# Optimization experiments

Hardware: AMD Instinct MI355X
Metric: run time of the kernel (lower is better)

The kernel has to match this reference:

```python
import jax, jax.numpy as jnp
import numpy as np

N_DOMAINS = 8
LN_EPS = 1e-5


def setup_inputs() -> dict:
    key = jax.random.key(0)
    ks = jax.random.split(key, 4)
    N, D_IN, D_HID, D_OUT = 32768, 256, 1024, 256
    x = jax.random.normal(ks[0], (N, D_IN), dtype=jnp.float32)
    domain_types = jax.random.randint(ks[1], (N,), 0, N_DOMAINS, dtype=jnp.int32)
    # Per-domain MLP parameters (8 independent experts)
    W1 = jax.random.normal(ks[2], (N_DOMAINS, D_IN, D_HID), dtype=jnp.float32) * (1.0 / np.sqrt(D_IN))
    b1 = jnp.zeros((N_DOMAINS, D_HID), dtype=jnp.float32)
    gamma = jnp.ones((N_DOMAINS, D_HID), dtype=jnp.float32)
    beta = jnp.zeros((N_DOMAINS, D_HID), dtype=jnp.float32)
    W2 = jax.random.normal(ks[3], (N_DOMAINS, D_HID, D_OUT), dtype=jnp.float32) * (1.0 / np.sqrt(D_HID))
    b2 = jnp.zeros((N_DOMAINS, D_OUT), dtype=jnp.float32)
    return {"x": x, "domain_types": domain_types, "W1": W1, "b1": b1,
            "gamma": gamma, "beta": beta, "W2": W2, "b2": b2}


def _expert_mlp(x, W1d, b1d, gd, bd, W2d, b2d):
    # Linear -> LayerNorm -> ReLU -> (Dropout: identity at eval) -> Linear
    h = x @ W1d + b1d                       # [N, hid]
    mu = jnp.mean(h, axis=-1, keepdims=True)
    var = jnp.mean(jnp.square(h - mu), axis=-1, keepdims=True)
    h = (h - mu) * jax.lax.rsqrt(var + LN_EPS) * gd + bd
    h = jax.nn.relu(h)
    return h @ W2d + b2d                    # [N, out]


def reference(x, domain_types, W1, b1, gamma, beta, W2, b2):
    # output dim == x.shape[-1] (as in the torch code: zeros(batch, x.shape[-1]))
    out = jnp.zeros((x.shape[0], x.shape[-1]), dtype=x.dtype)
    for d in range(N_DOMAINS):  # small fixed expert loop (static MoE dispatch)
        y = _expert_mlp(x, W1[d], b1[d], gamma[d], beta[d], W2[d], b2[d])
        mask = (domain_types == d)[:, None]
        out = jnp.where(mask, y, out)
    return out
```

## Files before the change

### kernel.cpp

```cpp
#include <hip/hip_runtime.h>
#include <hip/hip_bf16.h>


#define ND 8
#define NROWS 32768
#define DIN 256
#define DHID 1024
#define DOUT 256
#define MPAD 33792
#define NTILES 264

typedef short short8 __attribute__((ext_vector_type(8)));
typedef float floatx4 __attribute__((ext_vector_type(4)));

__device__ __forceinline__ unsigned short f2bf(float f) {
    unsigned u = __builtin_bit_cast(unsigned, f);
    unsigned r = u + 0x7fff + ((u >> 16) & 1);
    return (unsigned short)(r >> 16);
}
__device__ __forceinline__ float bf2f(unsigned short h) {
    unsigned u = ((unsigned)h) << 16;
    return __builtin_bit_cast(float, u);
}

#define GLDS16(gp, lp) __builtin_amdgcn_global_load_lds( \
    (const __attribute__((address_space(1))) void*)(gp), \
    (__attribute__((address_space(3))) void*)(lp), 16, 0, 0)

__global__ void transpose_bf16(const float* __restrict__ in,
                               unsigned short* __restrict__ out,
                               int R, int C) {
    __shared__ float t[32][33];
    const int z = blockIdx.z;
    const int c0 = blockIdx.x * 32, r0 = blockIdx.y * 32;
    const int tx = threadIdx.x & 31, ty = threadIdx.x >> 5;
    const float* src = in + (size_t)z * R * C;
    unsigned short* dst = out + (size_t)z * R * C;
#pragma unroll
    for (int i = 0; i < 32; i += 8)
        t[ty + i][tx] = src[(size_t)(r0 + ty + i) * C + c0 + tx];
    __syncthreads();
#pragma unroll
    for (int i = 0; i < 32; i += 8)
        dst[(size_t)(c0 + ty + i) * R + r0 + tx] = f2bf(t[tx][ty + i]);
}

__global__ void zero_init(int* __restrict__ perm, int* __restrict__ rowdom,
                          int* __restrict__ cnt) {
    int i = blockIdx.x * 256 + threadIdx.x;
    if (i < MPAD) { perm[i] = -1; rowdom[i] = 0; }
    if (i < 16) cnt[i] = 0;
}

__global__ void histo(const int* __restrict__ dt, int* __restrict__ counts) {
    __shared__ int lc[ND];
    if (threadIdx.x < ND) lc[threadIdx.x] = 0;
    __syncthreads();
    int i = blockIdx.x * 256 + threadIdx.x;
    atomicAdd(&lc[dt[i]], 1);
    __syncthreads();
    if (threadIdx.x < ND) atomicAdd(&counts[threadIdx.x], lc[threadIdx.x]);
}

__global__ void make_meta(const int* __restrict__ counts, int* __restrict__ cursors,
                          int2* __restrict__ meta) {
    if (threadIdx.x == 0 && blockIdx.x == 0) {
        int off = 0, t = 0;
        for (int d = 0; d < ND; d++) {
            cursors[d] = off;
            int nt = (counts[d] + 127) >> 7;
            for (int i = 0; i < nt; i++) meta[t++] = make_int2(d, off + (i << 7));
            off += nt << 7;
        }
        for (; t < NTILES; t++) meta[t] = make_int2(-1, 0);
    }
}

__global__ __launch_bounds__(256)
void assign_pos(const int* __restrict__ dt, int* __restrict__ cursors,
                int* __restrict__ perm, int* __restrict__ rowdom,
                int* __restrict__ pos) {
    __shared__ int lcnt[ND];
    __shared__ int lbase[ND];
    const int tid = threadIdx.x;
    if (tid < ND) lcnt[tid] = 0;
    __syncthreads();
    const int r = blockIdx.x * 256 + tid;
    const int d = dt[r];
    const int myrank = atomicAdd(&lcnt[d], 1);
    __syncthreads();
    if (tid < ND && lcnt[tid] > 0)
        lbase[tid] = atomicAdd(&cursors[tid], lcnt[tid]);
    __syncthreads();
    const int p = lbase[d] + myrank;
    pos[r] = p;
    perm[p] = r;
    rowdom[p] = d;
}

__global__ __launch_bounds__(256)
void copy_rows(const float* __restrict__ x, const int* __restrict__ pos,
               unsigned short* __restrict__ xs) {
    const int tid = threadIdx.x;
    const int lane = tid & 63;
    const int r = blockIdx.x * 4 + (tid >> 6);
    const int p = pos[r];
    float4 v = ((const float4*)(x + (size_t)r * DIN))[lane];
    ushort4 o;
    o.x = f2bf(v.x); o.y = f2bf(v.y); o.z = f2bf(v.z); o.w = f2bf(v.w);
    ((ushort4*)(xs + (size_t)p * DIN))[lane] = o;
}

template <int K, bool SCATTER>
__global__ __launch_bounds__(256, 2)
void gemm_bt(const unsigned short* __restrict__ A,
             const unsigned short* __restrict__ Bt,
             const float* __restrict__ bias,
             const int2* __restrict__ meta,
             const int* __restrict__ perm,
             unsigned short* __restrict__ Cbf,
             float* __restrict__ Cf,
             const int Ntot) {
    const int2 md = meta[blockIdx.x];
    const int dom = md.x;
    if (dom < 0) return;
    const int m0 = md.y;
    const int n0 = blockIdx.y * 128;

    __shared__ unsigned short As[128 * 32];
    __shared__ unsigned short Bs[128 * 32];

    const int tid = threadIdx.x;
    const int lane = tid & 63;
    const int w = tid >> 6;
    const int wr = w >> 1, wc = w & 1;

    const unsigned short* Abase = A + (size_t)m0 * K;
    const unsigned short* Bbase = Bt + (size_t)dom * Ntot * K + (size_t)n0 * K;

    floatx4 acc[4][4];
#pragma unroll
    for (int i = 0; i < 4; i++)
#pragma unroll
        for (int j = 0; j < 4; j++) acc[i][j] = 0.f;

    for (int k0 = 0; k0 < K; k0 += 32) {
#pragma unroll
        for (int it = 0; it < 2; ++it) {
            const int c = w * 128 + it * 64 + lane;
            const int m = c >> 2, kc = c & 3;
            GLDS16(Abase + (size_t)m * K + k0 + kc * 8, &As[(w * 128 + it * 64) * 8]);
            GLDS16(Bbase + (size_t)m * K + k0 + kc * 8, &Bs[(w * 128 + it * 64) * 8]);
        }
        __syncthreads();

        short8 a[4], b[4];
        const int kk = (lane >> 4) * 8;
#pragma unroll
        for (int i = 0; i < 4; i++) {
            const int m = wr * 64 + i * 16 + (lane & 15);
            a[i] = *(const short8*)&As[m * 32 + kk];
            const int n = wc * 64 + i * 16 + (lane & 15);
            b[i] = *(const short8*)&Bs[n * 32 + kk];
        }
#pragma unroll
        for (int i = 0; i < 4; i++)
#pragma unroll
            for (int j = 0; j < 4; j++)
                acc[i][j] = __builtin_amdgcn_mfma_f32_16x16x32_bf16(a[i], b[j], acc[i][j], 0, 0, 0);
        __syncthreads();
    }

    const int quad = lane >> 4;
#pragma unroll
    for (int i = 0; i < 4; i++) {
        const int rowbase = m0 + wr * 64 + i * 16 + quad * 4;
        if (!SCATTER) {
#pragma unroll
            for (int j = 0; j < 4; j++) {
                const int col = n0 + wc * 64 + j * 16 + (lane & 15);
                const float bv = bias[dom * Ntot + col];
#pragma unroll
                for (int r = 0; r < 4; r++)
                    Cbf[(size_t)(rowbase + r) * Ntot + col] = f2bf(acc[i][j][r] + bv);
            }
        } else {
#pragma unroll
            for (int r = 0; r < 4; r++) {
                const int orig = perm[rowbase + r];
                if (orig < 0) continue;
#pragma unroll
                for (int j = 0; j < 4; j++) {
                    const int col = n0 + wc * 64 + j * 16 + (lane & 15);
                    Cf[(size_t)orig * Ntot + col] = acc[i][j][r] + bias[dom * Ntot + col];
                }
            }
        }
    }
}

__global__ __launch_bounds__(256)
void ln_relu(unsigned short* __restrict__ H, const float* __restrict__ gamma,
             const float* __restrict__ beta, const int* __restrict__ rowdom) {
    const int row = blockIdx.x;
    const int tid = threadIdx.x;
    const int dom = rowdom[row];
    unsigned short* hr = H + (size_t)row * DHID;
    ushort4 raw = ((const ushort4*)hr)[tid];
    float v0 = bf2f(raw.x), v1 = bf2f(raw.y), v2 = bf2f(raw.z), v3 = bf2f(raw.w);
    float s = v0 + v1 + v2 + v3;
    float s2 = v0 * v0 + v1 * v1 + v2 * v2 + v3 * v3;
#pragma unroll
    for (int o = 32; o; o >>= 1) {
        s += __shfl_xor(s, o, 64);
        s2 += __shfl_xor(s2, o, 64);
    }
    __shared__ float red[8];
    const int w = tid >> 6;
    if ((tid & 63) == 0) { red[w] = s; red[4 + w] = s2; }
    __syncthreads();
    s = red[0] + red[1] + red[2] + red[3];
    s2 = red[4] + red[5] + red[6] + red[7];
    const float inv = 1.0f / 1024.0f;
    const float mu = s * inv;
    const float var = fmaxf(s2 * inv - mu * mu, 0.f);
    const float rstd = rsqrtf(var + 1e-5f);
    const float* g = gamma + dom * DHID + tid * 4;
    const float* b = beta + dom * DHID + tid * 4;
    ushort4 o4;
    o4.x = f2bf(fmaxf((v0 - mu) * rstd * g[0] + b[0], 0.f));
    o4.y = f2bf(fmaxf((v1 - mu) * rstd * g[1] + b[1], 0.f));
    o4.z = f2bf(fmaxf((v2 - mu) * rstd * g[2] + b[2], 0.f));
    o4.w = f2bf(fmaxf((v3 - mu) * rstd * g[3] + b[3], 0.f));
    ((ushort4*)hr)[tid] = o4;
}

extern "C" void kernel_launch(void* const* d_in, const int* in_sizes, int n_in,
                              void* d_out, int out_size, void* d_ws, size_t ws_size,
                              hipStream_t stream) {
    const float* x = (const float*)d_in[0];
    const int* dt = (const int*)d_in[1];
    const float* W1 = (const float*)d_in[2];
    const float* b1 = (const float*)d_in[3];
    const float* gamma = (const float*)d_in[4];
    const float* beta = (const float*)d_in[5];
    const float* W2 = (const float*)d_in[6];
    const float* b2 = (const float*)d_in[7];
    float* out = (float*)d_out;

    char* ws = (char*)d_ws;
    size_t off = 0;
    auto take = [&](size_t nbytes) -> char* {
        char* p = ws + off;
        off = (off + nbytes + 255) & ~(size_t)255;
        return p;
    };
    unsigned short* W1T = (unsigned short*)take((size_t)ND * DHID * DIN * 2);
    unsigned short* W2T = (unsigned short*)take((size_t)ND * DOUT * DHID * 2);
    unsigned short* XS  = (unsigned short*)take((size_t)MPAD * DIN * 2);
    unsigned short* H   = (unsigned short*)take((size_t)MPAD * DHID * 2);
    int* PERM   = (int*)take(MPAD * 4);
    int* ROWDOM = (int*)take(MPAD * 4);
    int* POS    = (int*)take(NROWS * 4);
    int* CNT    = (int*)take(64);
    int2* META  = (int2*)take(NTILES * 8);
    (void)ws_size; (void)n_in; (void)in_sizes; (void)out_size;

    int* COUNTS = CNT;
    int* CURSORS = CNT + 8;

    transpose_bf16<<<dim3(DHID / 32, DIN / 32, ND), 256, 0, stream>>>(W1, W1T, DIN, DHID);
    transpose_bf16<<<dim3(DOUT / 32, DHID / 32, ND), 256, 0, stream>>>(W2, W2T, DHID, DOUT);
    zero_init<<<(MPAD + 255) / 256, 256, 0, stream>>>(PERM, ROWDOM, CNT);
    histo<<<NROWS / 256, 256, 0, stream>>>(dt, COUNTS);
    make_meta<<<1, 1, 0, stream>>>(COUNTS, CURSORS, META);
    assign_pos<<<NROWS / 256, 256, 0, stream>>>(dt, CURSORS, PERM, ROWDOM, POS);
    copy_rows<<<NROWS / 4, 256, 0, stream>>>(x, POS, XS);
    gemm_bt<DIN, false><<<dim3(NTILES, DHID / 128), 256, 0, stream>>>(
        XS, W1T, b1, META, nullptr, H, nullptr, DHID);
    ln_relu<<<MPAD, 256, 0, stream>>>(H, gamma, beta, ROWDOM);
    gemm_bt<DHID, true><<<dim3(NTILES, DOUT / 128), 256, 0, stream>>>(
        H, W2T, b2, META, PERM, nullptr, out, DOUT);
}
```

Measured before the change: 227.4 us.

## Fuse first expert GEMM with LayerNorm+ReLU epilogue and drop zero-init kernel

Replaces the first GEMM and the separate LayerNorm/ReLU pass with one kernel. Each 512-thread block computes 64 rows across the full 1024 hidden columns, reduces mean and variance in the epilogue through shared memory, and writes the normalized bf16 activations once. This removes a full read-modify-write of the hidden buffer and a kernel launch. The zero_init kernel is also removed: counter reset moves into the transpose kernel and padding-row perm reset into make_meta. The wider block needs a large B tile in LDS (64 KB) and more accumulator registers, which may reduce occupancy. It also computes statistics from fp32 accumulators instead of bf16-rounded values.

```diff
diff --git a/kernel.cpp b/kernel.cpp
--- a/kernel.cpp
+++ b/kernel.cpp
@@ -29,11 +29,13 @@
 
 __global__ void transpose_bf16(const float* __restrict__ in,
                                unsigned short* __restrict__ out,
-                               int R, int C) {
+                               int R, int C, int* __restrict__ cnt) {
     __shared__ float t[32][33];
     const int z = blockIdx.z;
     const int c0 = blockIdx.x * 32, r0 = blockIdx.y * 32;
     const int tx = threadIdx.x & 31, ty = threadIdx.x >> 5;
+    if (cnt && blockIdx.x == 0 && blockIdx.y == 0 && z == 0 && threadIdx.x < 16)
+        cnt[threadIdx.x] = 0;
     const float* src = in + (size_t)z * R * C;
     unsigned short* dst = out + (size_t)z * R * C;
 #pragma unroll
@@ -43,13 +45,6 @@
 #pragma unroll
     for (int i = 0; i < 32; i += 8)
         dst[(size_t)(c0 + ty + i) * R + r0 + tx] = f2bf(t[tx][ty + i]);
-}
-
-__global__ void zero_init(int* __restrict__ perm, int* __restrict__ rowdom,
-                          int* __restrict__ cnt) {
-    int i = blockIdx.x * 256 + threadIdx.x;
-    if (i < MPAD) { perm[i] = -1; rowdom[i] = 0; }
-    if (i < 16) cnt[i] = 0;
 }
 
 __global__ void histo(const int* __restrict__ dt, int* __restrict__ counts) {
@@ -63,13 +58,14 @@
 }
 
 __global__ void make_meta(const int* __restrict__ counts, int* __restrict__ cursors,
-                          int2* __restrict__ meta) {
+                          int2* __restrict__ meta, int* __restrict__ perm) {
     if (threadIdx.x == 0 && blockIdx.x == 0) {
         int off = 0, t = 0;
         for (int d = 0; d < ND; d++) {
             cursors[d] = off;
             int nt = (counts[d] + 127) >> 7;
             for (int i = 0; i < nt; i++) meta[t++] = make_int2(d, off + (i << 7));
+            for (int p = off + counts[d]; p < off + (nt << 7); p++) perm[p] = -1;
             off += nt << 7;
         }
         for (; t < NTILES; t++) meta[t] = make_int2(-1, 0);
@@ -78,8 +74,7 @@
 
 __global__ __launch_bounds__(256)
 void assign_pos(const int* __restrict__ dt, int* __restrict__ cursors,
-                int* __restrict__ perm, int* __restrict__ rowdom,
-                int* __restrict__ pos) {
+                int* __restrict__ perm, int* __restrict__ pos) {
     __shared__ int lcnt[ND];
     __shared__ int lbase[ND];
     const int tid = threadIdx.x;
@@ -95,7 +90,6 @@
     const int p = lbase[d] + myrank;
     pos[r] = p;
     perm[p] = r;
-    rowdom[p] = d;
 }
 
 __global__ __launch_bounds__(256)
@@ -111,16 +105,141 @@
     ((ushort4*)(xs + (size_t)p * DIN))[lane] = o;
 }
 
-template <int K, bool SCATTER>
+__global__ __launch_bounds__(512, 2)
+void gemm_ln(const unsigned short* __restrict__ A,
+             const unsigned short* __restrict__ Bt,
+             const float* __restrict__ bias,
+             const float* __restrict__ gamma,
+             const float* __restrict__ beta,
+             const int2* __restrict__ meta,
+             unsigned short* __restrict__ H) {
+    const int2 md = meta[blockIdx.x >> 1];
+    const int dom = md.x;
+    if (dom < 0) return;
+    const int m0 = md.y + (blockIdx.x & 1) * 64;
+
+    __shared__ unsigned short As[64 * 32];
+    __shared__ unsigned short Bs[1024 * 32];
+    __shared__ float red_s[64][9];
+    __shared__ float red_q[64][9];
+    __shared__ float mu_s[64], rs_s[64];
+
+    const int tid = threadIdx.x;
+    const int lane = tid & 63;
+    const int w = tid >> 6;
+    const int c16 = lane & 15;
+    const int quad = lane >> 4;
+
+    const unsigned short* Abase = A + (size_t)m0 * DIN;
+    const unsigned short* Bbase = Bt + (size_t)dom * DHID * DIN;
+
+    floatx4 acc[4][8];
+#pragma unroll
+    for (int i = 0; i < 4; i++)
+#pragma unroll
+        for (int j = 0; j < 8; j++) acc[i][j] = 0.f;
+
+    for (int k0 = 0; k0 < DIN; k0 += 32) {
+#pragma unroll
+        for (int it = 0; it < 8; ++it) {
+            const int c = (w * 8 + it) * 64 + lane;
+            const int n = c >> 2, kc = c & 3;
+            GLDS16(Bbase + (size_t)n * DIN + k0 + kc * 8, &Bs[(w * 8 + it) * 512]);
+        }
+        if (w < 4) {
+            const int c = w * 64 + lane;
+            const int m = c >> 2, kc = c & 3;
+            GLDS16(Abase + (size_t)m * DIN + k0 + kc * 8, &As[w * 512]);
+        }
+        __syncthreads();
+
+        const int kk = quad * 8;
+        short8 a[4], b[8];
+#pragma unroll
+        for (int i = 0; i < 4; i++)
+            a[i] = *(const short8*)&As[(i * 16 + c16) * 32 + kk];
+#pragma unroll
+        for (int j = 0; j < 8; j++)
+            b[j] = *(const short8*)&Bs[(w * 128 + j * 16 + c16) * 32 + kk];
+#pragma unroll
+        for (int i = 0; i < 4; i++)
+#pragma unroll
+            for (int j = 0; j < 8; j++)
+                acc[i][j] = __builtin_amdgcn_mfma_f32_16x16x32_bf16(a[i], b[j], acc[i][j], 0, 0, 0);
+        __syncthreads();
+    }
+
+    float bv[8];
+#pragma unroll
+    for (int j = 0; j < 8; j++) bv[j] = bias[dom * DHID + w * 128 + j * 16 + c16];
+
+#pragma unroll
+    for (int i = 0; i < 4; i++) {
+#pragma unroll
+        for (int r = 0; r < 4; r++) {
+            float s = 0.f, q = 0.f;
+#pragma unroll
+            for (int j = 0; j < 8; j++) {
+                float v = acc[i][j][r] + bv[j];
+                acc[i][j][r] = v;
+                s += v; q += v * v;
+            }
+#pragma unroll
+            for (int o = 1; o < 16; o <<= 1) {
+                s += __shfl_xor(s, o, 64);
+                q += __shfl_xor(q, o, 64);
+            }
+            if (c16 == 0) {
+                const int row = i * 16 + quad * 4 + r;
+                red_s[row][w] = s;
+                red_q[row][w] = q;
+            }
+        }
+    }
+    __syncthreads();
+
+    if (tid < 64) {
+        float s = 0.f, q = 0.f;
+#pragma unroll
+        for (int ww = 0; ww < 8; ww++) { s += red_s[tid][ww]; q += red_q[tid][ww]; }
+        const float inv = 1.0f / (float)DHID;
+        const float mu = s * inv;
+        const float var = fmaxf(q * inv - mu * mu, 0.f);
+        mu_s[tid] = mu;
+        rs_s[tid] = rsqrtf(var + 1e-5f);
+    }
+    __syncthreads();
+
+    float gv[8], btv[8];
+#pragma unroll
+    for (int j = 0; j < 8; j++) {
+        gv[j] = gamma[dom * DHID + w * 128 + j * 16 + c16];
+        btv[j] = beta[dom * DHID + w * 128 + j * 16 + c16];
+    }
+#pragma unroll
+    for (int i = 0; i < 4; i++) {
+#pragma unroll
+        for (int r = 0; r < 4; r++) {
+            const int row = i * 16 + quad * 4 + r;
+            const float mu = mu_s[row], rs = rs_s[row];
+            unsigned short* hrow = H + (size_t)(m0 + row) * DHID + w * 128;
+#pragma unroll
+            for (int j = 0; j < 8; j++) {
+                float v = (acc[i][j][r] - mu) * rs * gv[j] + btv[j];
+                hrow[j * 16 + c16] = f2bf(fmaxf(v, 0.f));
+            }
+        }
+    }
+}
+
 __global__ __launch_bounds__(256, 2)
 void gemm_bt(const unsigned short* __restrict__ A,
              const unsigned short* __restrict__ Bt,
              const float* __restrict__ bias,
              const int2* __restrict__ meta,
              const int* __restrict__ perm,
-             unsigned short* __restrict__ Cbf,
              float* __restrict__ Cf,
-             const int Ntot) {
+             const int Ntot, const int K) {
     const int2 md = meta[blockIdx.x];
     const int dom = md.x;
     if (dom < 0) return;
@@ -175,64 +294,17 @@
 #pragma unroll
     for (int i = 0; i < 4; i++) {
         const int rowbase = m0 + wr * 64 + i * 16 + quad * 4;
-        if (!SCATTER) {
+#pragma unroll
+        for (int r = 0; r < 4; r++) {
+            const int orig = perm[rowbase + r];
+            if (orig < 0) continue;
 #pragma unroll
             for (int j = 0; j < 4; j++) {
                 const int col = n0 + wc * 64 + j * 16 + (lane & 15);
-                const float bv = bias[dom * Ntot + col];
-#pragma unroll
-                for (int r = 0; r < 4; r++)
-                    Cbf[(size_t)(rowbase + r) * Ntot + col] = f2bf(acc[i][j][r] + bv);
-            }
-        } else {
-#pragma unroll
-            for (int r = 0; r < 4; r++) {
-                const int orig = perm[rowbase + r];
-                if (orig < 0) continue;
-#pragma unroll
-                for (int j = 0; j < 4; j++) {
-                    const int col = n0 + wc * 64 + j * 16 + (lane & 15);
-                    Cf[(size_t)orig * Ntot + col] = acc[i][j][r] + bias[dom * Ntot + col];
-                }
-            }
-        }
-    }
-}
-
-__global__ __launch_bounds__(256)
-void ln_relu(unsigned short* __restrict__ H, const float* __restrict__ gamma,
-             const float* __restrict__ beta, const int* __restrict__ rowdom) {
-    const int row = blockIdx.x;
-    const int tid = threadIdx.x;
-    const int dom = rowdom[row];
-    unsigned short* hr = H + (size_t)row * DHID;
-    ushort4 raw = ((const ushort4*)hr)[tid];
-    float v0 = bf2f(raw.x), v1 = bf2f(raw.y), v2 = bf2f(raw.z), v3 = bf2f(raw.w);
-    float s = v0 + v1 + v2 + v3;
-    float s2 = v0 * v0 + v1 * v1 + v2 * v2 + v3 * v3;
-#pragma unroll
-    for (int o = 32; o; o >>= 1) {
-        s += __shfl_xor(s, o, 64);
-        s2 += __shfl_xor(s2, o, 64);
-    }
-    __shared__ float red[8];
-    const int w = tid >> 6;
-    if ((tid & 63) == 0) { red[w] = s; red[4 + w] = s2; }
-    __syncthreads();
-    s = red[0] + red[1] + red[2] + red[3];
-    s2 = red[4] + red[5] + red[6] + red[7];
-    const float inv = 1.0f / 1024.0f;
-    const float mu = s * inv;
-    const float var = fmaxf(s2 * inv - mu * mu, 0.f);
-    const float rstd = rsqrtf(var + 1e-5f);
-    const float* g = gamma + dom * DHID + tid * 4;
-    const float* b = beta + dom * DHID + tid * 4;
-    ushort4 o4;
-    o4.x = f2bf(fmaxf((v0 - mu) * rstd * g[0] + b[0], 0.f));
-    o4.y = f2bf(fmaxf((v1 - mu) * rstd * g[1] + b[1], 0.f));
-    o4.z = f2bf(fmaxf((v2 - mu) * rstd * g[2] + b[2], 0.f));
-    o4.w = f2bf(fmaxf((v3 - mu) * rstd * g[3] + b[3], 0.f));
-    ((ushort4*)hr)[tid] = o4;
+                Cf[(size_t)orig * Ntot + col] = acc[i][j][r] + bias[dom * Ntot + col];
+            }
+        }
+    }
 }
 
 extern "C" void kernel_launch(void* const* d_in, const int* in_sizes, int n_in,
@@ -260,7 +332,6 @@
     unsigned short* XS  = (unsigned short*)take((size_t)MPAD * DIN * 2);
     unsigned short* H   = (unsigned short*)take((size_t)MPAD * DHID * 2);
     int* PERM   = (int*)take(MPAD * 4);
-    int* ROWDOM = (int*)take(MPAD * 4);
     int* POS    = (int*)take(NROWS * 4);
     int* CNT    = (int*)take(64);
     int2* META  = (int2*)take(NTILES * 8);
@@ -269,16 +340,13 @@
     int* COUNTS = CNT;
     int* CURSORS = CNT + 8;
 
-    transpose_bf16<<<dim3(DHID / 32, DIN / 32, ND), 256, 0, stream>>>(W1, W1T, DIN, DHID);
-    transpose_bf16<<<dim3(DOUT / 32, DHID / 32, ND), 256, 0, stream>>>(W2, W2T, DHID, DOUT);
-    zero_init<<<(MPAD + 255) / 256, 256, 0, stream>>>(PERM, ROWDOM, CNT);
+    transpose_bf16<<<dim3(DHID / 32, DIN / 32, ND), 256, 0, stream>>>(W1, W1T, DIN, DHID, CNT);
+    transpose_bf16<<<dim3(DOUT / 32, DHID / 32, ND), 256, 0, stream>>>(W2, W2T, DHID, DOUT, nullptr);
     histo<<<NROWS / 256, 256, 0, stream>>>(dt, COUNTS);
-    make_meta<<<1, 1, 0, stream>>>(COUNTS, CURSORS, META);
-    assign_pos<<<NROWS / 256, 256, 0, stream>>>(dt, CURSORS, PERM, ROWDOM, POS);
+    make_meta<<<1, 1, 0, stream>>>(COUNTS, CURSORS, META, PERM);
+    assign_pos<<<NROWS / 256, 256, 0, stream>>>(dt, CURSORS, PERM, POS);
     copy_rows<<<NROWS / 4, 256, 0, stream>>>(x, POS, XS);
-    gemm_bt<DIN, false><<<dim3(NTILES, DHID / 128), 256, 0, stream>>>(
-        XS, W1T, b1, META, nullptr, H, nullptr, DHID);
-    ln_relu<<<MPAD, 256, 0, stream>>>(H, gamma, beta, ROWDOM);
-    gemm_bt<DHID, true><<<dim3(NTILES, DOUT / 128), 256, 0, stream>>>(
-        H, W2T, b2, META, PERM, nullptr, out, DOUT);
-}
+    gemm_ln<<<NTILES * 2, 512, 0, stream>>>(XS, W1T, b1, gamma, beta, META, H);
+    gemm_bt<<<dim3(NTILES, DOUT / 128), 256, 0, stream>>>(
+        H, W2T, b2, META, PERM, out, DOUT, DHID);
+}
```

New measurement: 247.8 us. +9.0%, slower.
